# Kernel tuning notes

Measured on AMD Instinct MI355X. Metric: run time of the kernel, lower is better.

## Reference

```python
import jax, jax.numpy as jnp
import numpy as np

D_MODEL = 512
NUM_HEADS = 8
D_K = D_MODEL // NUM_HEADS


def setup_inputs() -> dict:
    key = jax.random.key(0)
    k0, k1, k2, k3, k4 = jax.random.split(key, 5)
    s = 1.0 / np.sqrt(D_MODEL)
    return {
        "x": jax.random.normal(k0, (2, 4096, D_MODEL), dtype=jnp.float32),
        "W_q": jax.random.normal(k1, (D_MODEL, D_MODEL), dtype=jnp.float32) * s,
        "W_k": jax.random.normal(k2, (D_MODEL, D_MODEL), dtype=jnp.float32) * s,
        "W_v": jax.random.normal(k3, (D_MODEL, D_MODEL), dtype=jnp.float32) * s,
        "W_o": jax.random.normal(k4, (D_MODEL, D_MODEL), dtype=jnp.float32) * s,
    }


def reference(x, W_q, W_k, W_v, W_o):
    B, S, _ = x.shape
    # project and split heads: (B, H, S, d_k)
    def split(t):
        return t.reshape(B, S, NUM_HEADS, D_K).transpose(0, 2, 1, 3)
    Q = split(x @ W_q)
    K = split(x @ W_k)
    V = split(x @ W_v)
    scale = jnp.sqrt(jnp.asarray(D_K, dtype=x.dtype))
    logits = jnp.einsum('bhqd,bhkd->bhqk', Q, K) / scale
    attn = jax.nn.softmax(logits, axis=-1)  # dropout is identity at inference
    out = jnp.einsum('bhqk,bhkd->bhqd', attn, V)
    concat = out.transpose(0, 2, 1, 3).reshape(B, S, D_MODEL)
    return concat @ W_o
```

## Files before the change

kernel.cpp:

```cpp
#include <hip/hip_runtime.h>
#include <hip/hip_bf16.h>


#define DMODEL 512
#define SEQ    4096
#define NTOK   8192
#define LDQK   1024

using f32x4 = __attribute__((ext_vector_type(4))) float;
using s16x8 = __attribute__((ext_vector_type(8))) short;
using u16x8 = __attribute__((ext_vector_type(8))) unsigned short;

static __device__ __forceinline__ unsigned short f2bf(float f) {
  union { float f; unsigned u; } v; v.f = f;
  unsigned r = v.u + 0x7fff + ((v.u >> 16) & 1);
  return (unsigned short)(r >> 16);
}

static __device__ __forceinline__ unsigned pack_bf2(float lo, float hi) {
  __hip_bfloat162 t = __float22bfloat162_rn(make_float2(lo, hi));
  union { __hip_bfloat162 b; unsigned u; } c; c.b = t; return c.u;
}

static __device__ __forceinline__ void gll16(const void* g, void* l) {
  __builtin_amdgcn_global_load_lds(
      (const __attribute__((address_space(1))) unsigned int*)g,
      (__attribute__((address_space(3))) unsigned int*)l, 16, 0, 0);
}

__global__ void prep_kernel(const float* __restrict__ x,
                            const float* __restrict__ Wq,
                            const float* __restrict__ Wk,
                            const float* __restrict__ Wv,
                            const float* __restrict__ Wo,
                            unsigned short* __restrict__ xb,
                            unsigned short* __restrict__ Wall, float c2) {
  __shared__ float T[64][65];
  const int bx = blockIdx.x;
  if (bx < 1024) {
    for (int i = bx * 256 + threadIdx.x; i < NTOK * DMODEL / 4; i += 262144) {
      float4 v = ((const float4*)x)[i];
      ushort4 o;
      o.x = f2bf(v.x); o.y = f2bf(v.y); o.z = f2bf(v.z); o.w = f2bf(v.w);
      ((ushort4*)xb)[i] = o;
    }
    return;
  }
  const int t = bx - 1024;
  const int y = t >> 6, sub = t & 63;
  const float* W = (y == 0) ? Wq : (y == 1) ? Wk : (y == 2) ? Wv : Wo;
  const float scale = (y == 0) ? c2 : 1.0f;
  const int tk = (sub & 7) * 64;
  const int tn = (sub >> 3) * 64;
  const int r  = threadIdx.x >> 2;
  const int cq = threadIdx.x & 3;
#pragma unroll
  for (int i = 0; i < 4; ++i) {
    int c = (cq + 4 * i) * 4;
    float4 v = *(const float4*)&W[(size_t)(tk + r) * 512 + tn + c];
    T[r][c + 0] = v.x * scale; T[r][c + 1] = v.y * scale;
    T[r][c + 2] = v.z * scale; T[r][c + 3] = v.w * scale;
  }
  __syncthreads();
  const int n  = threadIdx.x >> 2;
  const int k0 = (threadIdx.x & 3) * 16;
#pragma unroll
  for (int j4 = 0; j4 < 4; ++j4) {
    ushort4 o;
    o.x = f2bf(T[k0 + j4 * 4 + 0][n]);
    o.y = f2bf(T[k0 + j4 * 4 + 1][n]);
    o.z = f2bf(T[k0 + j4 * 4 + 2][n]);
    o.w = f2bf(T[k0 + j4 * 4 + 3][n]);
    *(ushort4*)&Wall[(size_t)y * 262144 + (size_t)(tn + n) * 512 + tk + k0 + j4 * 4] = o;
  }
}

__global__ __launch_bounds__(256, 3) void gemm_qkv(
    const unsigned short* __restrict__ xb,
    const unsigned short* __restrict__ Wall,
    unsigned short* __restrict__ QKb,
    unsigned short* __restrict__ Vtb)
{
  __shared__ unsigned short As[128 * 32];
  __shared__ unsigned short Bs[128 * 32];
  const int by = blockIdx.y;
  const bool vmode = (by >= 8);
  const unsigned short* A  = vmode ? (Wall + 2 * 262144) : xb;
  const unsigned short* Bt = vmode ? xb : Wall;
  const size_t bm = vmode ? (size_t)(by - 8) * 128 : (size_t)blockIdx.x * 128;
  const size_t bn = vmode ? (size_t)blockIdx.x * 128 : (size_t)by * 128;
  const int tid  = threadIdx.x;
  const int wave = tid >> 6, lane = tid & 63;
  const int q4 = lane >> 4, ln = lane & 15;
  const int wm = (wave >> 1) * 64, wn = (wave & 1) * 64;
  f32x4 acc[4][4] = {};
  const int srow = wave * 16 + (lane >> 2);
  const int scol = (lane & 3) * 8;

  const unsigned short* Ag  = A  + (bm + srow)      * 512 + scol;
  const unsigned short* Ag2 = A  + (bm + 64 + srow) * 512 + scol;
  const unsigned short* Bg  = Bt + (bn + srow)      * 512 + scol;
  const unsigned short* Bg2 = Bt + (bn + 64 + srow) * 512 + scol;
  unsigned short* Ad  = As + wave * 512;
  unsigned short* Ad2 = As + 2048 + wave * 512;
  unsigned short* Bd  = Bs + wave * 512;
  unsigned short* Bd2 = Bs + 2048 + wave * 512;

  for (int kt = 0; kt < 512; kt += 32) {
    __syncthreads();
    gll16(Ag + kt,  Ad);
    gll16(Ag2 + kt, Ad2);
    gll16(Bg + kt,  Bd);
    gll16(Bg2 + kt, Bd2);
    __syncthreads();
    s16x8 af[4], bfr[4];
#pragma unroll
    for (int i = 0; i < 4; i++)
      af[i] = *(const s16x8*)(As + (wm + i * 16 + ln) * 32 + q4 * 8);
#pragma unroll
    for (int i = 0; i < 4; i++)
      bfr[i] = *(const s16x8*)(Bs + (wn + i * 16 + ln) * 32 + q4 * 8);
#pragma unroll
    for (int mi = 0; mi < 4; mi++)
#pragma unroll
      for (int ni = 0; ni < 4; ni++)
        acc[mi][ni] = __builtin_amdgcn_mfma_f32_16x16x32_bf16(
            af[mi], bfr[ni], acc[mi][ni], 0, 0, 0);
  }
#pragma unroll
  for (int mi = 0; mi < 4; mi++)
#pragma unroll
    for (int r = 0; r < 4; ++r) {
      size_t row = bm + wm + mi * 16 + q4 * 4 + r;
#pragma unroll
      for (int ni = 0; ni < 4; ni++) {
        size_t col = bn + wn + ni * 16 + ln;
        unsigned short hv = f2bf(acc[mi][ni][r]);
        if (!vmode) {
          QKb[row * 1024 + col] = hv;
        } else {
          int b = (int)(col >> 12), s = (int)(col & 4095);
          int sp = (s & ~63) | (s & 32) | (((s >> 2) & 3) << 3) |
                   (((s >> 4) & 1) << 2) | (s & 3);
          Vtb[(size_t)b * 2097152 + row * 4096 + sp] = hv;
        }
      }
    }
}

__global__ __launch_bounds__(256, 2) void attn_kernel(
    const unsigned short* __restrict__ QK,
    const unsigned short* __restrict__ Vt,
    unsigned short* __restrict__ Oc)
{
  const int bid = blockIdx.x + 32 * (blockIdx.y + 8 * blockIdx.z);
  const int lin = (bid & 7) * 64 + (bid >> 3);
  const int qt = lin & 31, bh = lin >> 5;
  const int h = bh & 7, b = bh >> 3;
  const int tid = threadIdx.x, wave = tid >> 6, lane = tid & 63;
  const int q4 = lane >> 4, ln = lane & 15;
  __shared__ unsigned short Ks[2][64 * 64];
  __shared__ unsigned short Vs[2][64 * 64];
  const size_t rowbase = (size_t)b * SEQ;
  const size_t qrow0   = (size_t)qt * 128 + wave * 32;
  const unsigned short* Kp  = QK + rowbase * LDQK + 512 + h * 64;
  const unsigned short* VTp = Vt + ((size_t)(b * 8 + h) * 64) * SEQ;

  s16x8 qf[2][2];
#pragma unroll
  for (int mf = 0; mf < 2; ++mf) {
    const unsigned short* q = QK + (rowbase + qrow0 + mf * 16 + ln) * LDQK + h * 64;
    qf[mf][0] = *(const s16x8*)(q + q4 * 8);
    qf[mf][1] = *(const s16x8*)(q + 32 + q4 * 8);
  }
  f32x4 o[2][4] = {};
  float lp[2] = {};

  const int srow = tid >> 2;
  const int c32  = (tid & 3) * 32;
  const int swz  = (srow & 7) << 4;
  const int wof0 = srow * 128 + ((c32 +  0) ^ swz);
  const int wof1 = srow * 128 + ((c32 + 16) ^ swz);
  const int rswz = (ln & 7) << 4;

  const unsigned short* kgp = Kp  + (size_t)srow * LDQK + (c32 >> 1);
  const unsigned short* vgp = VTp + (size_t)srow * SEQ + (c32 >> 1);

  u16x8 kr  = *(const u16x8*)kgp;
  u16x8 kr2 = *(const u16x8*)(kgp + 8);
  u16x8 vr  = *(const u16x8*)vgp;
  u16x8 vr2 = *(const u16x8*)(vgp + 8);
  *(u16x8*)((char*)Ks[0] + wof0) = kr;
  *(u16x8*)((char*)Ks[0] + wof1) = kr2;
  *(u16x8*)((char*)Vs[0] + wof0) = vr;
  *(u16x8*)((char*)Vs[0] + wof1) = vr2;
  kgp += (size_t)64 * LDQK;  vgp += 64;
  kr  = *(const u16x8*)kgp;
  kr2 = *(const u16x8*)(kgp + 8);
  vr  = *(const u16x8*)vgp;
  vr2 = *(const u16x8*)(vgp + 8);
  __syncthreads();

  const f32x4 fz = {0.f, 0.f, 0.f, 0.f};

  for (int t = 0; t < 64; ++t) {
    const int cur = t & 1;
    const char* Kc = (const char*)Ks[cur];
    const char* Vc = (const char*)Vs[cur];

    f32x4 s4[2][4];
#pragma unroll
    for (int ni = 0; ni < 4; ni++) {
      const char* kb = Kc + (ni * 16 + ln) * 128;
      s16x8 kf0 = *(const s16x8*)(kb + ((q4 * 16)      ^ rswz));
      s16x8 kf1 = *(const s16x8*)(kb + ((q4 * 16 + 64) ^ rswz));
      __builtin_amdgcn_s_setprio(1);
#pragma unroll
      for (int mf = 0; mf < 2; ++mf) {
        f32x4 acc0 = __builtin_amdgcn_mfma_f32_16x16x32_bf16(kf0, qf[mf][0], fz, 0, 0, 0);
        s4[mf][ni] = __builtin_amdgcn_mfma_f32_16x16x32_bf16(kf1, qf[mf][1], acc0, 0, 0, 0);
      }
      __builtin_amdgcn_s_setprio(0);
    }
    s16x8 vf[2][4];
#pragma unroll
    for (int ks = 0; ks < 2; ++ks)
#pragma unroll
      for (int ni = 0; ni < 4; ni++)
        vf[ks][ni] = *(const s16x8*)(Vc + (ni * 16 + ln) * 128 +
                                     ((ks * 64 + q4 * 16) ^ rswz));

    s16x8 pf[2][2];
#pragma unroll
    for (int mf = 0; mf < 2; ++mf) {
      float e[4][4];
#pragma unroll
      for (int ni = 0; ni < 4; ni++)
#pragma unroll
        for (int r = 0; r < 4; ++r)
          e[ni][r] = __builtin_amdgcn_exp2f(s4[mf][ni][r]);
      float t0 = (e[0][0] + e[0][1]) + (e[0][2] + e[0][3]);
      float t1 = (e[1][0] + e[1][1]) + (e[1][2] + e[1][3]);
      float t2 = (e[2][0] + e[2][1]) + (e[2][2] + e[2][3]);
      float t3 = (e[3][0] + e[3][1]) + (e[3][2] + e[3][3]);
      lp[mf] += (t0 + t1) + (t2 + t3);
#pragma unroll
      for (int ks = 0; ks < 2; ++ks) {
        union { s16x8 v; unsigned u[4]; } pu;
        pu.u[0] = pack_bf2(e[2 * ks][0],     e[2 * ks][1]);
        pu.u[1] = pack_bf2(e[2 * ks][2],     e[2 * ks][3]);
        pu.u[2] = pack_bf2(e[2 * ks + 1][0], e[2 * ks + 1][1]);
        pu.u[3] = pack_bf2(e[2 * ks + 1][2], e[2 * ks + 1][3]);
        pf[mf][ks] = pu.v;
      }
    }
    __builtin_amdgcn_s_setprio(1);
#pragma unroll
    for (int ks = 0; ks < 2; ++ks)
#pragma unroll
      for (int ni = 0; ni < 4; ni++)
#pragma unroll
        for (int mf = 0; mf < 2; ++mf)
          o[mf][ni] = __builtin_amdgcn_mfma_f32_16x16x32_bf16(pf[mf][ks], vf[ks][ni], o[mf][ni], 0, 0, 0);
    __builtin_amdgcn_s_setprio(0);

    if (t + 1 < 64) {
      char* Kn = (char*)Ks[cur ^ 1];
      char* Vn = (char*)Vs[cur ^ 1];
      *(u16x8*)(Kn + wof0) = kr;
      *(u16x8*)(Kn + wof1) = kr2;
      *(u16x8*)(Vn + wof0) = vr;
      *(u16x8*)(Vn + wof1) = vr2;
      if (t + 2 < 64) {
        kgp += (size_t)64 * LDQK;  vgp += 64;
        kr  = *(const u16x8*)kgp;
        kr2 = *(const u16x8*)(kgp + 8);
        vr  = *(const u16x8*)vgp;
        vr2 = *(const u16x8*)(vgp + 8);
      }
    }
    __syncthreads();
  }
#pragma unroll
  for (int mf = 0; mf < 2; ++mf) {
    float l = lp[mf];
    l += __shfl_xor(l, 16, 64);
    l += __shfl_xor(l, 32, 64);
    const float inv = 1.0f / l;
#pragma unroll
    for (int r = 0; r < 4; ++r) {
      const float nv = __shfl(inv, q4 * 4 + r, 64);
      const size_t row = rowbase + qrow0 + mf * 16 + q4 * 4 + r;
#pragma unroll
      for (int ni = 0; ni < 4; ni++)
        Oc[row * 512 + h * 64 + ni * 16 + ln] = f2bf(o[mf][ni][r] * nv);
    }
  }
}

__global__ __launch_bounds__(256, 3) void gemm_out(
    const unsigned short* __restrict__ A,
    const unsigned short* __restrict__ Bt,
    float* __restrict__ C)
{
  __shared__ unsigned short As[128 * 32];
  __shared__ unsigned short Bs[64 * 32];
  const int tid  = threadIdx.x;
  const int wave = tid >> 6, lane = tid & 63;
  const int q4 = lane >> 4, ln = lane & 15;
  const size_t bm = (size_t)blockIdx.x * 128;
  const size_t bn = (size_t)blockIdx.y * 64;
  const int wm = (wave >> 1) * 64, wn = (wave & 1) * 32;
  f32x4 acc[4][2] = {};
  const int srow = wave * 16 + (lane >> 2);
  const int scol = (lane & 3) * 8;

  const unsigned short* Ag  = A  + (bm + srow)      * 512 + scol;
  const unsigned short* Ag2 = A  + (bm + 64 + srow) * 512 + scol;
  const unsigned short* Bg  = Bt + (bn + srow)      * 512 + scol;
  unsigned short* Ad  = As + wave * 512;
  unsigned short* Ad2 = As + 2048 + wave * 512;
  unsigned short* Bd  = Bs + wave * 512;

  for (int kt = 0; kt < 512; kt += 32) {
    __syncthreads();
    gll16(Ag + kt,  Ad);
    gll16(Ag2 + kt, Ad2);
    gll16(Bg + kt,  Bd);
    __syncthreads();
    s16x8 af[4], bfr[2];
#pragma unroll
    for (int i = 0; i < 4; i++)
      af[i] = *(const s16x8*)(As + (wm + i * 16 + ln) * 32 + q4 * 8);
#pragma unroll
    for (int i = 0; i < 2; i++)
      bfr[i] = *(const s16x8*)(Bs + (wn + i * 16 + ln) * 32 + q4 * 8);
#pragma unroll
    for (int mi = 0; mi < 4; mi++)
#pragma unroll
      for (int ni = 0; ni < 2; ni++)
        acc[mi][ni] = __builtin_amdgcn_mfma_f32_16x16x32_bf16(
            af[mi], bfr[ni], acc[mi][ni], 0, 0, 0);
  }
#pragma unroll
  for (int mi = 0; mi < 4; mi++)
#pragma unroll
    for (int r = 0; r < 4; ++r) {
      size_t row = bm + wm + mi * 16 + q4 * 4 + r;
#pragma unroll
      for (int ni = 0; ni < 2; ni++)
        C[row * 512 + bn + wn + ni * 16 + ln] = acc[mi][ni][r];
    }
}

extern "C" void kernel_launch(void* const* d_in, const int* in_sizes, int n_in,
                              void* d_out, int out_size, void* d_ws, size_t ws_size,
                              hipStream_t stream) {
  const float* x  = (const float*)d_in[0];
  const float* Wq = (const float*)d_in[1];
  const float* Wk = (const float*)d_in[2];
  const float* Wv = (const float*)d_in[3];
  const float* Wo = (const float*)d_in[4];

  char* ws = (char*)d_ws;
  unsigned short* xb    = (unsigned short*)(ws);
  unsigned short* Wall  = (unsigned short*)(ws + 8388608);
  unsigned short* QKb   = (unsigned short*)(ws + 10485760);
  unsigned short* Vtb   = (unsigned short*)(ws + 27262976);
  unsigned short* Oc    = (unsigned short*)(ws + 35651584);

  const float C2 = 0.125f * 1.44269504088896f;

  hipLaunchKernelGGL(prep_kernel, dim3(1280), dim3(256), 0, stream,
                     x, Wq, Wk, Wv, Wo, xb, Wall, C2);
  hipLaunchKernelGGL(gemm_qkv, dim3(64, 12), dim3(256), 0, stream,
                     xb, Wall, QKb, Vtb);
  hipLaunchKernelGGL(attn_kernel, dim3(32, 8, 2), dim3(256), 0, stream,
                     QKb, Vtb, Oc);
  hipLaunchKernelGGL(gemm_out, dim3(64, 8), dim3(256), 0, stream,
                     Oc, Wall + 3 * 262144, (float*)d_out);
}
```

Before: 191.0 us.

## Software-pipeline attention loop so PV MFMA of previous tile overlaps current softmax

```diff
diff --git a/kernel.cpp b/kernel.cpp
--- a/kernel.cpp
+++ b/kernel.cpp
@@ -203,11 +203,12 @@
 
   const f32x4 fz = {0.f, 0.f, 0.f, 0.f};
 
-  for (int t = 0; t < 64; ++t) {
-    const int cur = t & 1;
-    const char* Kc = (const char*)Ks[cur];
-    const char* Vc = (const char*)Vs[cur];
-
+  s16x8 vfp[2][4];
+  s16x8 pfp[2][2];
+
+  {
+    const char* Kc = (const char*)Ks[0];
+    const char* Vc = (const char*)Vs[0];
     f32x4 s4[2][4];
 #pragma unroll
     for (int ni = 0; ni < 4; ni++) {
@@ -222,15 +223,12 @@
       }
       __builtin_amdgcn_s_setprio(0);
     }
-    s16x8 vf[2][4];
 #pragma unroll
     for (int ks = 0; ks < 2; ++ks)
 #pragma unroll
       for (int ni = 0; ni < 4; ni++)
-        vf[ks][ni] = *(const s16x8*)(Vc + (ni * 16 + ln) * 128 +
-                                     ((ks * 64 + q4 * 16) ^ rswz));
-
-    s16x8 pf[2][2];
+        vfp[ks][ni] = *(const s16x8*)(Vc + (ni * 16 + ln) * 128 +
+                                      ((ks * 64 + q4 * 16) ^ rswz));
 #pragma unroll
     for (int mf = 0; mf < 2; ++mf) {
       float e[4][4];
@@ -251,18 +249,83 @@
         pu.u[1] = pack_bf2(e[2 * ks][2],     e[2 * ks][3]);
         pu.u[2] = pack_bf2(e[2 * ks + 1][0], e[2 * ks + 1][1]);
         pu.u[3] = pack_bf2(e[2 * ks + 1][2], e[2 * ks + 1][3]);
-        pf[mf][ks] = pu.v;
-      }
-    }
-    __builtin_amdgcn_s_setprio(1);
+        pfp[mf][ks] = pu.v;
+      }
+    }
+    char* Kn = (char*)Ks[1];
+    char* Vn = (char*)Vs[1];
+    *(u16x8*)(Kn + wof0) = kr;
+    *(u16x8*)(Kn + wof1) = kr2;
+    *(u16x8*)(Vn + wof0) = vr;
+    *(u16x8*)(Vn + wof1) = vr2;
+    kgp += (size_t)64 * LDQK;  vgp += 64;
+    kr  = *(const u16x8*)kgp;
+    kr2 = *(const u16x8*)(kgp + 8);
+    vr  = *(const u16x8*)vgp;
+    vr2 = *(const u16x8*)(vgp + 8);
+    __syncthreads();
+  }
+
+  for (int t = 1; t < 64; ++t) {
+    const int cur = t & 1;
+    const char* Kc = (const char*)Ks[cur];
+    const char* Vc = (const char*)Vs[cur];
+
+    f32x4 s4[2][4];
+#pragma unroll
+    for (int ni = 0; ni < 4; ni++) {
+      const char* kb = Kc + (ni * 16 + ln) * 128;
+      s16x8 kf0 = *(const s16x8*)(kb + ((q4 * 16)      ^ rswz));
+      s16x8 kf1 = *(const s16x8*)(kb + ((q4 * 16 + 64) ^ rswz));
+      __builtin_amdgcn_s_setprio(1);
+#pragma unroll
+      for (int mf = 0; mf < 2; ++mf) {
+        f32x4 acc0 = __builtin_amdgcn_mfma_f32_16x16x32_bf16(kf0, qf[mf][0], fz, 0, 0, 0);
+        s4[mf][ni] = __builtin_amdgcn_mfma_f32_16x16x32_bf16(kf1, qf[mf][1], acc0, 0, 0, 0);
+      }
+      __builtin_amdgcn_s_setprio(0);
+    }
+
 #pragma unroll
     for (int ks = 0; ks < 2; ++ks)
 #pragma unroll
       for (int ni = 0; ni < 4; ni++)
 #pragma unroll
         for (int mf = 0; mf < 2; ++mf)
-          o[mf][ni] = __builtin_amdgcn_mfma_f32_16x16x32_bf16(pf[mf][ks], vf[ks][ni], o[mf][ni], 0, 0, 0);
-    __builtin_amdgcn_s_setprio(0);
+          o[mf][ni] = __builtin_amdgcn_mfma_f32_16x16x32_bf16(pfp[mf][ks], vfp[ks][ni], o[mf][ni], 0, 0, 0);
+
+    s16x8 vfc[2][4];
+#pragma unroll
+    for (int ks = 0; ks < 2; ++ks)
+#pragma unroll
+      for (int ni = 0; ni < 4; ni++)
+        vfc[ks][ni] = *(const s16x8*)(Vc + (ni * 16 + ln) * 128 +
+                                      ((ks * 64 + q4 * 16) ^ rswz));
+
+    s16x8 pfc[2][2];
+#pragma unroll
+    for (int mf = 0; mf < 2; ++mf) {
+      float e[4][4];
+#pragma unroll
+      for (int ni = 0; ni < 4; ni++)
+#pragma unroll
+        for (int r = 0; r < 4; ++r)
+          e[ni][r] = __builtin_amdgcn_exp2f(s4[mf][ni][r]);
+      float t0 = (e[0][0] + e[0][1]) + (e[0][2] + e[0][3]);
+      float t1 = (e[1][0] + e[1][1]) + (e[1][2] + e[1][3]);
+      float t2 = (e[2][0] + e[2][1]) + (e[2][2] + e[2][3]);
+      float t3 = (e[3][0] + e[3][1]) + (e[3][2] + e[3][3]);
+      lp[mf] += (t0 + t1) + (t2 + t3);
+#pragma unroll
+      for (int ks = 0; ks < 2; ++ks) {
+        union { s16x8 v; unsigned u[4]; } pu;
+        pu.u[0] = pack_bf2(e[2 * ks][0],     e[2 * ks][1]);
+        pu.u[1] = pack_bf2(e[2 * ks][2],     e[2 * ks][3]);
+        pu.u[2] = pack_bf2(e[2 * ks + 1][0], e[2 * ks + 1][1]);
+        pu.u[3] = pack_bf2(e[2 * ks + 1][2], e[2 * ks + 1][3]);
+        pfc[mf][ks] = pu.v;
+      }
+    }
 
     if (t + 1 < 64) {
       char* Kn = (char*)Ks[cur ^ 1];
@@ -279,8 +342,31 @@
         vr2 = *(const u16x8*)(vgp + 8);
       }
     }
-    __syncthreads();
-  }
+
+#pragma unroll
+    for (int ks = 0; ks < 2; ++ks)
+#pragma unroll
+      for (int ni = 0; ni < 4; ni++)
+        vfp[ks][ni] = vfc[ks][ni];
+#pragma unroll
+    for (int mf = 0; mf < 2; ++mf)
+#pragma unroll
+      for (int ks = 0; ks < 2; ++ks)
+        pfp[mf][ks] = pfc[mf][ks];
+
+    __syncthreads();
+  }
+
+  __builtin_amdgcn_s_setprio(1);
+#pragma unroll
+  for (int ks = 0; ks < 2; ++ks)
+#pragma unroll
+    for (int ni = 0; ni < 4; ni++)
+#pragma unroll
+      for (int mf = 0; mf < 2; ++mf)
+        o[mf][ni] = __builtin_amdgcn_mfma_f32_16x16x32_bf16(pfp[mf][ks], vfp[ks][ni], o[mf][ni], 0, 0, 0);
+  __builtin_amdgcn_s_setprio(0);
+
 #pragma unroll
   for (int mf = 0; mf < 2; ++mf) {
     float l = lp[mf];
```

After: 185.4 us. 1.03x faster.
